# Optimization experiments

Measured on AMD Instinct MI355X. Metric: run time of the kernel, lower is better.

Reference implementation:

```python
import jax, jax.numpy as jnp
import numpy as np

N = 262144   # occupied voxels
H = 64       # channels
G = 128      # dense grid extent per axis (coords in [0, G))
K = 27       # 3x3x3 kernel offsets


def _build_neighbor_map():
    rng = np.random.default_rng(0)
    lin = rng.choice(G ** 3, size=N, replace=False).astype(np.int64)
    coords = np.stack(np.unravel_index(lin, (G, G, G)), axis=1)  # [N,3]
    table = np.full(G ** 3, N, dtype=np.int32)  # sentinel N -> zero row
    table[lin] = np.arange(N, dtype=np.int32)
    offs = np.array([(dx, dy, dz) for dx in (-1, 0, 1)
                     for dy in (-1, 0, 1) for dz in (-1, 0, 1)], dtype=np.int64)
    nbr = np.full((N, K), N, dtype=np.int32)
    for k in range(K):
        nc = coords + offs[k]
        ok = np.all((nc >= 0) & (nc < G), axis=1)
        nl = nc[ok, 0] * G * G + nc[ok, 1] * G + nc[ok, 2]
        nbr[ok, k] = table[nl]
    return nbr


def setup_inputs() -> dict:
    key = jax.random.key(0)
    k1, k2, k3 = jax.random.split(key, 3)
    scale = 1.0 / np.sqrt(K * H)  # ME-style fan-in init scale
    x = jax.random.normal(k1, (N, H), dtype=jnp.float32)
    Wa = jax.random.normal(k2, (K, H, H), dtype=jnp.float32) * scale
    Wb = jax.random.normal(k3, (K, H, H), dtype=jnp.float32) * scale
    nbr = jnp.asarray(_build_neighbor_map())
    return {"x": x, "Wa": Wa, "Wb": Wb, "nbr": nbr}


def _sparse_conv(feats, W, nbr):
    # gather -> GEMM -> accumulate, per kernel offset (missing neighbors hit zero row)
    fpad = jnp.concatenate([feats, jnp.zeros((1, feats.shape[1]), feats.dtype)], axis=0)
    out = jnp.zeros((feats.shape[0], W.shape[2]), feats.dtype)
    for k in range(W.shape[0]):
        out = out + fpad[nbr[:, k]] @ W[k]
    return out


def reference(x, Wa, Wb, nbr):
    out = _sparse_conv(x, Wa, nbr)          # spconva
    out = jax.nn.relu(out)                  # MinkowskiReLU
    out = _sparse_conv(out, Wb, nbr)        # spconvb
    return out + x                          # residual add
```

## Files before the change

### kernel.cpp

```cpp
#include <hip/hip_runtime.h>


#define N_ROWS 262144
#define HCH    64
#define KOFF   27
#define CHUNK  3

typedef unsigned short u16;
typedef __attribute__((ext_vector_type(8))) short short8;
typedef __attribute__((ext_vector_type(4))) float f32x4;

__device__ __forceinline__ u16 f2bf(float f) {
    unsigned u = __builtin_bit_cast(unsigned, f);
    unsigned r = (u + 0x7FFFu + ((u >> 16) & 1u)) >> 16;
    return (u16)r;
}
__device__ __forceinline__ float bf2f(u16 h) {
    return __builtin_bit_cast(float, (unsigned)h << 16);
}
__device__ __forceinline__ unsigned pack2(float a, float b) {
    return (unsigned)f2bf(a) | ((unsigned)f2bf(b) << 16);
}

__global__ void prep_all(const float* __restrict__ x, u16* __restrict__ xb,
                         u16* __restrict__ yb,
                         const float* __restrict__ Wa, const float* __restrict__ Wb,
                         u16* __restrict__ Wta, u16* __restrict__ Wtb,
                         const int* __restrict__ nbr, int* __restrict__ nbrT) {
    const int b = blockIdx.x;
    if (b < 8193) {
        long gid = (long)b * 256 + threadIdx.x;
        const long total = (long)N_ROWS * HCH / 8;
        if (gid < total) {
            const float4* s = (const float4*)(x + gid * 8);
            float4 a = s[0], c = s[1];
            uint4 v;
            v.x = pack2(a.x, a.y); v.y = pack2(a.z, a.w);
            v.z = pack2(c.x, c.y); v.w = pack2(c.z, c.w);
            *(uint4*)(xb + gid * 8) = v;
        } else if (gid < total + HCH / 8) {
            long c = gid - total;
            uint4 z; z.x = 0; z.y = 0; z.z = 0; z.w = 0;
            *(uint4*)(xb + (long)N_ROWS * HCH + c * 8) = z;
            *(uint4*)(yb + (long)N_ROWS * HCH + c * 8) = z;
        }
    } else if (b < 9057) {
        int gid = (b - 8193) * 256 + threadIdx.x;
        const int total = KOFF * HCH * HCH;
        const float* src; u16* dst; int e;
        if (gid < total)          { src = Wa; dst = Wta; e = gid; }
        else if (gid < 2 * total) { src = Wb; dst = Wtb; e = gid - total; }
        else return;
        int k = e >> 12, i = (e >> 6) & 63, j = e & 63;
        dst[(k << 12) + (j << 6) + i] = f2bf(src[e]);
    } else {
        __shared__ int t[256 * 27];
        const int rowbase = (b - 9057) * 256;
        for (int e = threadIdx.x; e < 256 * 27; e += 256)
            t[e] = nbr[(size_t)rowbase * KOFF + e];
        __syncthreads();
        for (int e = threadIdx.x; e < 256 * 27; e += 256) {
            int k = e >> 8, r = e & 255;
            nbrT[(size_t)k * N_ROWS + rowbase + r] = t[r * KOFF + k];
        }
    }
}

template <bool FIRST>
__global__ __launch_bounds__(256, 2) void conv_kernel(
    const u16* __restrict__ xg,
    const u16* __restrict__ Wt,
    const int* __restrict__ nb,
    u16* __restrict__ ybf,
    float* __restrict__ outf,
    const u16* __restrict__ residb)
{
    __shared__ uint4 Wlds4[2 * CHUNK * 512];
    float* Fsh = (float*)Wlds4;

    const int tid  = threadIdx.x;
    const int wave = tid >> 6;
    const int lane = tid & 63;
    const int m    = lane & 15;
    const int q    = lane >> 4;
    const int base = blockIdx.x * 256 + wave * 64;

    int row[4];
#pragma unroll
    for (int t = 0; t < 4; t++) row[t] = base + t * 16 + m;

    auto ld_idx = [&](int k, int t) -> int {
        return nb[(size_t)k * N_ROWS + row[t]];
    };

    auto ldA = [&](int idx, short8& a0, short8& a1) {
        short8 z = {0, 0, 0, 0, 0, 0, 0, 0};
        a0 = z; a1 = z;
        if (idx != N_ROWS) {
            const u16* ar = xg + (size_t)idx * HCH + q * 8;
            a0 = *(const short8*)ar;
            a1 = *(const short8*)(ar + 32);
        }
    };

    auto stageW = [&](int c, int bufSel) {
        const char* gbase = (const char*)(Wt + (size_t)c * CHUNK * 4096);
        uint4* bufBase = Wlds4 + bufSel * (CHUNK * 512);
#pragma unroll
        for (int i = 0; i < 6; i++) {
            int p = i * 256 + wave * 64 + lane;
            int e = (p & ~7) | ((p & 7) ^ ((p >> 3) & 7));
            const unsigned* src = (const unsigned*)(gbase + (size_t)e * 16);
            unsigned* dst = (unsigned*)(bufBase + i * 256 + wave * 64);
            __builtin_amdgcn_global_load_lds(
                (const __attribute__((address_space(1))) unsigned*)src,
                (__attribute__((address_space(3))) unsigned*)dst,
                16, 0, 0);
        }
    };

    f32x4 acc[4][4];
#pragma unroll
    for (int t = 0; t < 4; t++)
#pragma unroll
        for (int jt = 0; jt < 4; jt++)
            acc[t][jt] = (f32x4){0.f, 0.f, 0.f, 0.f};

    stageW(0, 0);

    int i0[4], i1[4], idxRing[2][4];
#pragma unroll
    for (int t = 0; t < 4; t++) i0[t] = ld_idx(0, t);
#pragma unroll
    for (int t = 0; t < 4; t++) i1[t] = ld_idx(1, t);
#pragma unroll
    for (int t = 0; t < 4; t++) idxRing[0][t] = ld_idx(2, t);
#pragma unroll
    for (int t = 0; t < 4; t++) idxRing[1][t] = ld_idx(3, t);

    short8 Aring[3][4][2];
#pragma unroll
    for (int t = 0; t < 4; t++) ldA(i0[t], Aring[0][t][0], Aring[0][t][1]);
#pragma unroll
    for (int t = 0; t < 4; t++) ldA(i1[t], Aring[1][t][0], Aring[1][t][1]);

    __syncthreads();

#pragma unroll
    for (int c = 0; c < KOFF / CHUNK; c++) {
        const int buf = c & 1;
        if (c + 1 < KOFF / CHUNK) stageW(c + 1, buf ^ 1);

        const u16* WshC = (const u16*)(Wlds4 + buf * (CHUNK * 512));
#pragma unroll
        for (int s = 0; s < CHUNK; s++) {
            const int kk  = c * CHUNK + s;
            const int par = kk & 1;
            const int cur = kk % 3;
            const int nxt = (kk + 2) % 3;

#pragma unroll
            for (int t = 0; t < 4; t++)
                ldA(idxRing[par][t], Aring[nxt][t][0], Aring[nxt][t][1]);
            const int k4 = (kk + 4 < KOFF) ? kk + 4 : KOFF - 1;
#pragma unroll
            for (int t = 0; t < 4; t++) idxRing[par][t] = ld_idx(k4, t);

            const u16* bs = WshC + s * 4096;
            short8 B0[4], B1[4];
#pragma unroll
            for (int jt = 0; jt < 4; jt++) {
                int j = jt * 16 + m;
                B0[jt] = *(const short8*)(bs + j * 64 + ((q    ) ^ (m & 7)) * 8);
                B1[jt] = *(const short8*)(bs + j * 64 + ((q + 4) ^ (m & 7)) * 8);
            }

#pragma unroll
            for (int t = 0; t < 4; t++)
#pragma unroll
                for (int jt = 0; jt < 4; jt++)
                    acc[t][jt] = __builtin_amdgcn_mfma_f32_16x16x32_bf16(
                        Aring[cur][t][0], B0[jt], acc[t][jt], 0, 0, 0);
#pragma unroll
            for (int t = 0; t < 4; t++)
#pragma unroll
                for (int jt = 0; jt < 4; jt++)
                    acc[t][jt] = __builtin_amdgcn_mfma_f32_16x16x32_bf16(
                        Aring[cur][t][1], B1[jt], acc[t][jt], 0, 0, 0);
        }

        __syncthreads();
    }

    float* sl = Fsh + wave * (16 * 68);
    const int r = lane & 15;
    const int h = lane >> 4;
#pragma unroll
    for (int t = 0; t < 4; t++) {
        __syncthreads();
#pragma unroll
        for (int jt = 0; jt < 4; jt++)
#pragma unroll
            for (int rr = 0; rr < 4; rr++)
                sl[(q * 4 + rr) * 68 + jt * 16 + m] = acc[t][jt][rr];
        __syncthreads();

        float4 v0 = *(const float4*)&sl[r * 68 + h * 16 + 0];
        float4 v1 = *(const float4*)&sl[r * 68 + h * 16 + 4];
        float4 v2 = *(const float4*)&sl[r * 68 + h * 16 + 8];
        float4 v3 = *(const float4*)&sl[r * 68 + h * 16 + 12];
        const size_t grow = (size_t)(base + t * 16 + r);
        if (FIRST) {
            uint4 o0, o1;
            o0.x = pack2(fmaxf(v0.x, 0.f), fmaxf(v0.y, 0.f));
            o0.y = pack2(fmaxf(v0.z, 0.f), fmaxf(v0.w, 0.f));
            o0.z = pack2(fmaxf(v1.x, 0.f), fmaxf(v1.y, 0.f));
            o0.w = pack2(fmaxf(v1.z, 0.f), fmaxf(v1.w, 0.f));
            o1.x = pack2(fmaxf(v2.x, 0.f), fmaxf(v2.y, 0.f));
            o1.y = pack2(fmaxf(v2.z, 0.f), fmaxf(v2.w, 0.f));
            o1.z = pack2(fmaxf(v3.x, 0.f), fmaxf(v3.y, 0.f));
            o1.w = pack2(fmaxf(v3.z, 0.f), fmaxf(v3.w, 0.f));
            uint4* dst = (uint4*)(ybf + grow * HCH + h * 16);
            dst[0] = o0; dst[1] = o1;
        } else {
            const uint4* rb = (const uint4*)(residb + grow * HCH + h * 16);
            uint4 r0 = rb[0], r1 = rb[1];
            float4 o;
            float* op = outf + grow * HCH + h * 16;
            o.x = v0.x + bf2f((u16)(r0.x & 0xFFFF));
            o.y = v0.y + bf2f((u16)(r0.x >> 16));
            o.z = v0.z + bf2f((u16)(r0.y & 0xFFFF));
            o.w = v0.w + bf2f((u16)(r0.y >> 16));
            *(float4*)(op + 0) = o;
            o.x = v1.x + bf2f((u16)(r0.z & 0xFFFF));
            o.y = v1.y + bf2f((u16)(r0.z >> 16));
            o.z = v1.z + bf2f((u16)(r0.w & 0xFFFF));
            o.w = v1.w + bf2f((u16)(r0.w >> 16));
            *(float4*)(op + 4) = o;
            o.x = v2.x + bf2f((u16)(r1.x & 0xFFFF));
            o.y = v2.y + bf2f((u16)(r1.x >> 16));
            o.z = v2.z + bf2f((u16)(r1.y & 0xFFFF));
            o.w = v2.w + bf2f((u16)(r1.y >> 16));
            *(float4*)(op + 8) = o;
            o.x = v3.x + bf2f((u16)(r1.z & 0xFFFF));
            o.y = v3.y + bf2f((u16)(r1.z >> 16));
            o.z = v3.z + bf2f((u16)(r1.w & 0xFFFF));
            o.w = v3.w + bf2f((u16)(r1.w >> 16));
            *(float4*)(op + 12) = o;
        }
    }
}

extern "C" void kernel_launch(void* const* d_in, const int* in_sizes, int n_in,
                              void* d_out, int out_size, void* d_ws, size_t ws_size,
                              hipStream_t stream) {
    const float* x   = (const float*)d_in[0];
    const float* Wa  = (const float*)d_in[1];
    const float* Wb  = (const float*)d_in[2];
    const int*   nbr = (const int*)d_in[3];
    float* out = (float*)d_out;

    char* ws = (char*)d_ws;
    const size_t xb_bytes = (size_t)(N_ROWS + 1) * HCH * sizeof(u16);
    const size_t w_bytes  = (size_t)KOFF * HCH * HCH * sizeof(u16);
    u16* xb  = (u16*)ws;
    u16* yb  = (u16*)(ws + xb_bytes);
    u16* Wta = (u16*)(ws + 2 * xb_bytes);
    u16* Wtb = (u16*)(ws + 2 * xb_bytes + w_bytes);
    int* nbrT = (int*)(ws + 2 * xb_bytes + 2 * w_bytes);

    prep_all<<<10081, 256, 0, stream>>>(x, xb, yb, Wa, Wb, Wta, Wtb, nbr, nbrT);
    conv_kernel<true ><<<N_ROWS / 256, 256, 0, stream>>>(xb, Wta, nbrT, yb, nullptr, nullptr);
    conv_kernel<false><<<N_ROWS / 256, 256, 0, stream>>>(yb, Wtb, nbrT, nullptr, out, xb);
}
```

Baseline: 274.8 us.

## Stage gathered neighbor rows into LDS via async global_load_lds ring

Replaces the per-lane register gather of neighbor feature rows with asynchronous global_load_lds into a three-slot LDS ring per wave, using swizzled layout and shuffled indices so each lane issues full 16-byte row segments. Index loads are now one coalesced load per lane instead of four strided ones. Missing neighbors are handled by zero-filling LDS before the loads. The kernel uses much more LDS and launch bounds drop to one block per SIMD pair, lowering occupancy, and the explicit vmcnt waits may serialize more than before.

```diff
diff --git a/kernel.cpp b/kernel.cpp
--- a/kernel.cpp
+++ b/kernel.cpp
@@ -67,7 +67,7 @@
 }
 
 template <bool FIRST>
-__global__ __launch_bounds__(256, 2) void conv_kernel(
+__global__ __launch_bounds__(256, 1) void conv_kernel(
     const u16* __restrict__ xg,
     const u16* __restrict__ Wt,
     const int* __restrict__ nb,
@@ -76,6 +76,7 @@
     const u16* __restrict__ residb)
 {
     __shared__ uint4 Wlds4[2 * CHUNK * 512];
+    __shared__ uint4 Alds[3][4][512];
     float* Fsh = (float*)Wlds4;
 
     const int tid  = threadIdx.x;
@@ -85,23 +86,8 @@
     const int q    = lane >> 4;
     const int base = blockIdx.x * 256 + wave * 64;
 
-    int row[4];
-#pragma unroll
-    for (int t = 0; t < 4; t++) row[t] = base + t * 16 + m;
-
-    auto ld_idx = [&](int k, int t) -> int {
-        return nb[(size_t)k * N_ROWS + row[t]];
-    };
-
-    auto ldA = [&](int idx, short8& a0, short8& a1) {
-        short8 z = {0, 0, 0, 0, 0, 0, 0, 0};
-        a0 = z; a1 = z;
-        if (idx != N_ROWS) {
-            const u16* ar = xg + (size_t)idx * HCH + q * 8;
-            a0 = *(const short8*)ar;
-            a1 = *(const short8*)(ar + 32);
-        }
-    };
+    const int coffE = (((lane & 7) ^ (lane >> 3)) << 3);
+    const int rsub  = lane >> 3;
 
     auto stageW = [&](int c, int bufSel) {
         const char* gbase = (const char*)(Wt + (size_t)c * CHUNK * 4096);
@@ -119,6 +105,27 @@
         }
     };
 
+    auto stageA = [&](int slot, int iv) {
+        uint4* Ab4 = &Alds[slot][wave][0];
+        uint4 z; z.x = 0; z.y = 0; z.z = 0; z.w = 0;
+#pragma unroll
+        for (int i = 0; i < 8; i++) Ab4[i * 64 + lane] = z;
+        asm volatile("s_waitcnt lgkmcnt(0)" ::: "memory");
+        char* Ab = (char*)Ab4;
+#pragma unroll
+        for (int g = 0; g < 8; g++) {
+            int idxr = __shfl(iv, g * 8 + rsub, 64);
+            if (idxr != N_ROWS) {
+                const u16* src = xg + (size_t)idxr * HCH + coffE;
+                unsigned* dst = (unsigned*)(Ab + g * 1024);
+                __builtin_amdgcn_global_load_lds(
+                    (const __attribute__((address_space(1))) unsigned*)src,
+                    (__attribute__((address_space(3))) unsigned*)dst,
+                    16, 0, 0);
+            }
+        }
+    };
+
     f32x4 acc[4][4];
 #pragma unroll
     for (int t = 0; t < 4; t++)
@@ -127,44 +134,32 @@
             acc[t][jt] = (f32x4){0.f, 0.f, 0.f, 0.f};
 
     stageW(0, 0);
-
-    int i0[4], i1[4], idxRing[2][4];
-#pragma unroll
-    for (int t = 0; t < 4; t++) i0[t] = ld_idx(0, t);
-#pragma unroll
-    for (int t = 0; t < 4; t++) i1[t] = ld_idx(1, t);
-#pragma unroll
-    for (int t = 0; t < 4; t++) idxRing[0][t] = ld_idx(2, t);
-#pragma unroll
-    for (int t = 0; t < 4; t++) idxRing[1][t] = ld_idx(3, t);
-
-    short8 Aring[3][4][2];
-#pragma unroll
-    for (int t = 0; t < 4; t++) ldA(i0[t], Aring[0][t][0], Aring[0][t][1]);
-#pragma unroll
-    for (int t = 0; t < 4; t++) ldA(i1[t], Aring[1][t][0], Aring[1][t][1]);
-
+    int iv0 = nb[base + lane];
+    int iv1 = nb[(size_t)1 * N_ROWS + base + lane];
+    int ivP[2];
+    ivP[0] = nb[(size_t)2 * N_ROWS + base + lane];
+    ivP[1] = nb[(size_t)3 * N_ROWS + base + lane];
+    stageA(0, iv0);
+    stageA(1, iv1);
     __syncthreads();
 
 #pragma unroll
     for (int c = 0; c < KOFF / CHUNK; c++) {
-        const int buf = c & 1;
-        if (c + 1 < KOFF / CHUNK) stageW(c + 1, buf ^ 1);
-
-        const u16* WshC = (const u16*)(Wlds4 + buf * (CHUNK * 512));
+        const int wbuf = c & 1;
+        if (c + 1 < KOFF / CHUNK) stageW(c + 1, wbuf ^ 1);
+
+        const u16* WshC = (const u16*)(Wlds4 + wbuf * (CHUNK * 512));
 #pragma unroll
         for (int s = 0; s < CHUNK; s++) {
-            const int kk  = c * CHUNK + s;
-            const int par = kk & 1;
-            const int cur = kk % 3;
-            const int nxt = (kk + 2) % 3;
-
-#pragma unroll
-            for (int t = 0; t < 4; t++)
-                ldA(idxRing[par][t], Aring[nxt][t][0], Aring[nxt][t][1]);
-            const int k4 = (kk + 4 < KOFF) ? kk + 4 : KOFF - 1;
-#pragma unroll
-            for (int t = 0; t < 4; t++) idxRing[par][t] = ld_idx(k4, t);
+            const int kk = c * CHUNK + s;
+
+            if (s == 2) asm volatile("s_waitcnt vmcnt(0)" ::: "memory");
+
+            if (kk + 2 < KOFF) {
+                stageA((kk + 2) % 3, ivP[kk & 1]);
+                const int k4 = (kk + 4 < KOFF) ? kk + 4 : KOFF - 1;
+                ivP[kk & 1] = nb[(size_t)k4 * N_ROWS + base + lane];
+            }
 
             const u16* bs = WshC + s * 4096;
             short8 B0[4], B1[4];
@@ -175,18 +170,27 @@
                 B1[jt] = *(const short8*)(bs + j * 64 + ((q + 4) ^ (m & 7)) * 8);
             }
 
+            const u16* Ar = (const u16*)&Alds[kk % 3][wave][0];
+            short8 A0[4], A1[4];
+#pragma unroll
+            for (int t = 0; t < 4; t++) {
+                int r = t * 16 + m;
+                A0[t] = *(const short8*)(Ar + r * 64 + ((q       ^ (r & 7)) << 3));
+                A1[t] = *(const short8*)(Ar + r * 64 + (((q + 4) ^ (r & 7)) << 3));
+            }
+
 #pragma unroll
             for (int t = 0; t < 4; t++)
 #pragma unroll
                 for (int jt = 0; jt < 4; jt++)
                     acc[t][jt] = __builtin_amdgcn_mfma_f32_16x16x32_bf16(
-                        Aring[cur][t][0], B0[jt], acc[t][jt], 0, 0, 0);
+                        A0[t], B0[jt], acc[t][jt], 0, 0, 0);
 #pragma unroll
             for (int t = 0; t < 4; t++)
 #pragma unroll
                 for (int jt = 0; jt < 4; jt++)
                     acc[t][jt] = __builtin_amdgcn_mfma_f32_16x16x32_bf16(
-                        Aring[cur][t][1], B1[jt], acc[t][jt], 0, 0, 0);
+                        A1[t], B1[jt], acc[t][jt], 0, 0, 0);
         }
 
         __syncthreads();
```

Result: slower. 447.6 us (+62.9%).

## Drop the neighbor-map transpose and stage per-block indices in LDS

Applied to the files above, without the earlier changes.

Removes the prep pass that transposed the neighbor map into k-major order. Each conv block now copies its contiguous 256×27 slice of the original row-major map into shared memory with vector loads, and reads gather indices from there. The old register ring of prefetched indices goes away. This avoids a full read and write of the index map and the scattered per-offset global index loads. The cost is about 27 KB of extra LDS per block, which could limit occupancy, plus a cooperative copy at kernel start.

```diff
diff --git a/kernel.cpp b/kernel.cpp
--- a/kernel.cpp
+++ b/kernel.cpp
@@ -25,8 +25,7 @@
 __global__ void prep_all(const float* __restrict__ x, u16* __restrict__ xb,
                          u16* __restrict__ yb,
                          const float* __restrict__ Wa, const float* __restrict__ Wb,
-                         u16* __restrict__ Wta, u16* __restrict__ Wtb,
-                         const int* __restrict__ nbr, int* __restrict__ nbrT) {
+                         u16* __restrict__ Wta, u16* __restrict__ Wtb) {
     const int b = blockIdx.x;
     if (b < 8193) {
         long gid = (long)b * 256 + threadIdx.x;
@@ -44,7 +43,7 @@
             *(uint4*)(xb + (long)N_ROWS * HCH + c * 8) = z;
             *(uint4*)(yb + (long)N_ROWS * HCH + c * 8) = z;
         }
-    } else if (b < 9057) {
+    } else {
         int gid = (b - 8193) * 256 + threadIdx.x;
         const int total = KOFF * HCH * HCH;
         const float* src; u16* dst; int e;
@@ -53,16 +52,6 @@
         else return;
         int k = e >> 12, i = (e >> 6) & 63, j = e & 63;
         dst[(k << 12) + (j << 6) + i] = f2bf(src[e]);
-    } else {
-        __shared__ int t[256 * 27];
-        const int rowbase = (b - 9057) * 256;
-        for (int e = threadIdx.x; e < 256 * 27; e += 256)
-            t[e] = nbr[(size_t)rowbase * KOFF + e];
-        __syncthreads();
-        for (int e = threadIdx.x; e < 256 * 27; e += 256) {
-            int k = e >> 8, r = e & 255;
-            nbrT[(size_t)k * N_ROWS + rowbase + r] = t[r * KOFF + k];
-        }
     }
 }
 
@@ -70,12 +59,13 @@
 __global__ __launch_bounds__(256, 2) void conv_kernel(
     const u16* __restrict__ xg,
     const u16* __restrict__ Wt,
-    const int* __restrict__ nb,
+    const int* __restrict__ nbr,
     u16* __restrict__ ybf,
     float* __restrict__ outf,
     const u16* __restrict__ residb)
 {
     __shared__ uint4 Wlds4[2 * CHUNK * 512];
+    __shared__ int   ilds[256 * KOFF];
     float* Fsh = (float*)Wlds4;
 
     const int tid  = threadIdx.x;
@@ -85,13 +75,9 @@
     const int q    = lane >> 4;
     const int base = blockIdx.x * 256 + wave * 64;
 
-    int row[4];
-#pragma unroll
-    for (int t = 0; t < 4; t++) row[t] = base + t * 16 + m;
-
-    auto ld_idx = [&](int k, int t) -> int {
-        return nb[(size_t)k * N_ROWS + row[t]];
-    };
+    int lrow[4];
+#pragma unroll
+    for (int t = 0; t < 4; t++) lrow[t] = wave * 64 + t * 16 + m;
 
     auto ldA = [&](int idx, short8& a0, short8& a1) {
         short8 z = {0, 0, 0, 0, 0, 0, 0, 0};
@@ -127,16 +113,19 @@
             acc[t][jt] = (f32x4){0.f, 0.f, 0.f, 0.f};
 
     stageW(0, 0);
-
-    int i0[4], i1[4], idxRing[2][4];
-#pragma unroll
-    for (int t = 0; t < 4; t++) i0[t] = ld_idx(0, t);
-#pragma unroll
-    for (int t = 0; t < 4; t++) i1[t] = ld_idx(1, t);
-#pragma unroll
-    for (int t = 0; t < 4; t++) idxRing[0][t] = ld_idx(2, t);
-#pragma unroll
-    for (int t = 0; t < 4; t++) idxRing[1][t] = ld_idx(3, t);
+    {
+        const uint4* g = (const uint4*)(nbr + (size_t)blockIdx.x * 256 * KOFF);
+        uint4* d = (uint4*)ilds;
+        for (int e = tid; e < 256 * KOFF / 4; e += 256) d[e] = g[e];
+    }
+
+    int i0[4], i1[4];
+#pragma unroll
+    for (int t = 0; t < 4; t++)
+        i0[t] = nbr[(size_t)(blockIdx.x * 256 + lrow[t]) * KOFF + 0];
+#pragma unroll
+    for (int t = 0; t < 4; t++)
+        i1[t] = nbr[(size_t)(blockIdx.x * 256 + lrow[t]) * KOFF + 1];
 
     short8 Aring[3][4][2];
 #pragma unroll
@@ -155,16 +144,16 @@
 #pragma unroll
         for (int s = 0; s < CHUNK; s++) {
             const int kk  = c * CHUNK + s;
-            const int par = kk & 1;
             const int cur = kk % 3;
             const int nxt = (kk + 2) % 3;
 
-#pragma unroll
-            for (int t = 0; t < 4; t++)
-                ldA(idxRing[par][t], Aring[nxt][t][0], Aring[nxt][t][1]);
-            const int k4 = (kk + 4 < KOFF) ? kk + 4 : KOFF - 1;
-#pragma unroll
-            for (int t = 0; t < 4; t++) idxRing[par][t] = ld_idx(k4, t);
+            if (kk + 2 < KOFF) {
+#pragma unroll
+                for (int t = 0; t < 4; t++) {
+                    int id2 = ilds[lrow[t] * KOFF + (kk + 2)];
+                    ldA(id2, Aring[nxt][t][0], Aring[nxt][t][1]);
+                }
+            }
 
             const u16* bs = WshC + s * 4096;
             short8 B0[4], B1[4];
@@ -267,9 +256,8 @@
     u16* yb  = (u16*)(ws + xb_bytes);
     u16* Wta = (u16*)(ws + 2 * xb_bytes);
     u16* Wtb = (u16*)(ws + 2 * xb_bytes + w_bytes);
-    int* nbrT = (int*)(ws + 2 * xb_bytes + 2 * w_bytes);
-
-    prep_all<<<10081, 256, 0, stream>>>(x, xb, yb, Wa, Wb, Wta, Wtb, nbr, nbrT);
-    conv_kernel<true ><<<N_ROWS / 256, 256, 0, stream>>>(xb, Wta, nbrT, yb, nullptr, nullptr);
-    conv_kernel<false><<<N_ROWS / 256, 256, 0, stream>>>(yb, Wtb, nbrT, nullptr, out, xb);
-}
+
+    prep_all<<<9057, 256, 0, stream>>>(x, xb, yb, Wa, Wb, Wta, Wtb);
+    conv_kernel<true ><<<N_ROWS / 256, 256, 0, stream>>>(xb, Wta, nbr, yb, nullptr, nullptr);
+    conv_kernel<false><<<N_ROWS / 256, 256, 0, stream>>>(yb, Wtb, nbr, nullptr, out, xb);
+}
```

Result: faster. 263.0 us (-4.3%).
